# Kernel optimization log

Measured on AMD Instinct MI355X. Metric: run time of the kernel, lower is better.

Reference implementation:

```python
import jax, jax.numpy as jnp
import numpy as np

D_IN, D_MODEL = 512, 256
B, N = 2, 512


def setup_inputs() -> dict:
    key = jax.random.key(0)
    ks = jax.random.split(key, 8)
    xav_x = float(np.sqrt(2.0 / (D_IN + D_MODEL)))
    xav_p = float(np.sqrt(2.0 / (4 + D_MODEL)))
    return {
        "x": jax.random.normal(ks[0], (B, N, D_IN), dtype=jnp.float32),
        "pos": jax.random.normal(ks[1], (B, N, 4), dtype=jnp.float32),
        "attn_mask": jax.random.randint(ks[2], (B, N, N), 0, 2, dtype=jnp.int32),
        "Wx": jax.random.normal(ks[3], (D_IN, D_MODEL), dtype=jnp.float32) * xav_x,
        "bx": jnp.zeros((D_MODEL,), dtype=jnp.float32),
        "Wp": jax.random.normal(ks[4], (4, D_MODEL), dtype=jnp.float32) * xav_p,
        "bp": jnp.zeros((D_MODEL,), dtype=jnp.float32),
        "w": jax.random.normal(ks[5], (D_MODEL,), dtype=jnp.float32) * 0.05,
    }


def reference(x, pos, attn_mask, Wx, bx, Wp, bp, w):
    # projected, activated inputs: [B, N, d_model]
    h = jnp.tanh(x @ Wx + bx)
    # pairwise relative positions: [B, N, N, 4]
    rel = pos[:, :, None, :] - pos[:, None, :, :]
    # position MLP + tanh: [B, N, N, d_model]
    z = jnp.tanh(rel @ Wp + bp)
    # scores via dot with weight vector: [B, N, N]
    attn = jnp.einsum("bijd,d->bij", z, w)
    mask = attn_mask != 0
    attn = jnp.where(mask, attn, -jnp.inf)
    attn = jax.nn.softmax(attn, axis=2)
    attn = jnp.where(mask, attn, 0.0)
    # dropout is identity in eval mode
    # weighted sum: [B, N, d_model]
    output = jnp.einsum("bij,bjd->bid", attn, h)
    return (output, attn)
```

## Files before the change

### kernel.cpp

```cpp
#include <hip/hip_runtime.h>
#include <hip/hip_bf16.h>
#include <math.h>

#define BATCH   2
#define SEQ     512
#define DIN     512
#define DM      256

#define LOG2E2  2.88539008177792681f

#if __has_builtin(__builtin_amdgcn_exp2f)
#define EXP2(x) __builtin_amdgcn_exp2f(x)
#else
#define EXP2(x) exp2f(x)
#endif
#if __has_builtin(__builtin_amdgcn_rcpf)
#define RCP(x) __builtin_amdgcn_rcpf(x)
#else
#define RCP(x) (1.0f / (x))
#endif

__device__ __forceinline__ float tanh_from_scaled(float targ) {
    return fmaf(-2.0f, RCP(1.0f + EXP2(targ)), 1.0f);
}

__global__ __launch_bounds__(512) void prep_k(
    const float* __restrict__ pos,
    const float* __restrict__ Wp,
    const float* __restrict__ bp,
    const float* __restrict__ x,
    const float* __restrict__ Wx,
    const float* __restrict__ bx,
    float* __restrict__ EA,
    float2* __restrict__ EB2,
    float* __restrict__ h)
{
    const int tid = threadIdx.x;

    if (blockIdx.x < 256) {
        const int b  = blockIdx.x >> 7;
        const int tg = blockIdx.x & 127;
        const int d0 = 2 * tg, d1 = d0 + 1;

        const float4 p = ((const float4*)pos)[b * SEQ + tid];
        const float P0 = fmaf(p.x, Wp[d0], fmaf(p.y, Wp[DM + d0],
                         fmaf(p.z, Wp[2*DM + d0], p.w * Wp[3*DM + d0])));
        const float P1 = fmaf(p.x, Wp[d1], fmaf(p.y, Wp[DM + d1],
                         fmaf(p.z, Wp[2*DM + d1], p.w * Wp[3*DM + d1])));
        EB2[((size_t)(b * 128 + tg)) * SEQ + tid] =
            make_float2(EXP2(-LOG2E2 * P0), EXP2(-LOG2E2 * P1));
        return;
    }

    __shared__ float4 s_x[2][DIN/4];
    __shared__ float4 s_part[2][7][64];

    const int row0 = (blockIdx.x - 256) * 2;

    {
        const int r2  = __builtin_amdgcn_readfirstlane(tid >> 8);
        const int d   = tid & 255;
        const int row = row0 + r2;
        const float4 p = ((const float4*)pos)[row];
        const float P = fmaf(p.x, Wp[d],
                        fmaf(p.y, Wp[DM + d],
                        fmaf(p.z, Wp[2*DM + d],
                             p.w * Wp[3*DM + d])));
        EA[(size_t)row * DM + d] = EXP2(LOG2E2 * (P + bp[d]));
    }

    if (tid < 256) {
        const int r   = tid >> 7;
        const int idx = tid & 127;
        s_x[r][idx] = ((const float4*)(x + (size_t)(row0 + r) * DIN))[idx];
    }
    __syncthreads();

    const int w = tid >> 6;
    const int l = tid & 63;

    float4 acc0 = make_float4(0.f, 0.f, 0.f, 0.f);
    float4 acc1 = make_float4(0.f, 0.f, 0.f, 0.f);
    const float* __restrict__ wxp = Wx + 4 * l;

    #pragma unroll 2
    for (int k4 = 0; k4 < 16; k4++) {
        const int kk = w * 16 + k4;
        const float4 xv0 = s_x[0][kk];
        const float4 xv1 = s_x[1][kk];
        const float4 w0 = *(const float4*)(wxp + (size_t)(4*kk + 0) * DM);
        const float4 w1 = *(const float4*)(wxp + (size_t)(4*kk + 1) * DM);
        const float4 w2 = *(const float4*)(wxp + (size_t)(4*kk + 2) * DM);
        const float4 w3 = *(const float4*)(wxp + (size_t)(4*kk + 3) * DM);
        acc0.x = fmaf(xv0.x, w0.x, acc0.x); acc0.y = fmaf(xv0.x, w0.y, acc0.y);
        acc0.z = fmaf(xv0.x, w0.z, acc0.z); acc0.w = fmaf(xv0.x, w0.w, acc0.w);
        acc0.x = fmaf(xv0.y, w1.x, acc0.x); acc0.y = fmaf(xv0.y, w1.y, acc0.y);
        acc0.z = fmaf(xv0.y, w1.z, acc0.z); acc0.w = fmaf(xv0.y, w1.w, acc0.w);
        acc0.x = fmaf(xv0.z, w2.x, acc0.x); acc0.y = fmaf(xv0.z, w2.y, acc0.y);
        acc0.z = fmaf(xv0.z, w2.z, acc0.z); acc0.w = fmaf(xv0.z, w2.w, acc0.w);
        acc0.x = fmaf(xv0.w, w3.x, acc0.x); acc0.y = fmaf(xv0.w, w3.y, acc0.y);
        acc0.z = fmaf(xv0.w, w3.z, acc0.z); acc0.w = fmaf(xv0.w, w3.w, acc0.w);
        acc1.x = fmaf(xv1.x, w0.x, acc1.x); acc1.y = fmaf(xv1.x, w0.y, acc1.y);
        acc1.z = fmaf(xv1.x, w0.z, acc1.z); acc1.w = fmaf(xv1.x, w0.w, acc1.w);
        acc1.x = fmaf(xv1.y, w1.x, acc1.x); acc1.y = fmaf(xv1.y, w1.y, acc1.y);
        acc1.z = fmaf(xv1.y, w1.z, acc1.z); acc1.w = fmaf(xv1.y, w1.w, acc1.w);
        acc1.x = fmaf(xv1.z, w2.x, acc1.x); acc1.y = fmaf(xv1.z, w2.y, acc1.y);
        acc1.z = fmaf(xv1.z, w2.z, acc1.z); acc1.w = fmaf(xv1.z, w2.w, acc1.w);
        acc1.x = fmaf(xv1.w, w3.x, acc1.x); acc1.y = fmaf(xv1.w, w3.y, acc1.y);
        acc1.z = fmaf(xv1.w, w3.z, acc1.z); acc1.w = fmaf(xv1.w, w3.w, acc1.w);
    }

    if (w) {
        s_part[0][w - 1][l] = acc0;
        s_part[1][w - 1][l] = acc1;
    }
    __syncthreads();
    if (w == 0) {
        const float4 b4 = ((const float4*)bx)[l];
        acc0.x += b4.x; acc0.y += b4.y; acc0.z += b4.z; acc0.w += b4.w;
        acc1.x += b4.x; acc1.y += b4.y; acc1.z += b4.z; acc1.w += b4.w;
        #pragma unroll
        for (int q = 0; q < 7; q++) {
            const float4 q0 = s_part[0][q][l];
            const float4 q1 = s_part[1][q][l];
            acc0.x += q0.x; acc0.y += q0.y; acc0.z += q0.z; acc0.w += q0.w;
            acc1.x += q1.x; acc1.y += q1.y; acc1.z += q1.z; acc1.w += q1.w;
        }
        float4 t0, t1;
        t0.x = tanh_from_scaled(LOG2E2 * acc0.x);
        t0.y = tanh_from_scaled(LOG2E2 * acc0.y);
        t0.z = tanh_from_scaled(LOG2E2 * acc0.z);
        t0.w = tanh_from_scaled(LOG2E2 * acc0.w);
        t1.x = tanh_from_scaled(LOG2E2 * acc1.x);
        t1.y = tanh_from_scaled(LOG2E2 * acc1.y);
        t1.z = tanh_from_scaled(LOG2E2 * acc1.z);
        t1.w = tanh_from_scaled(LOG2E2 * acc1.w);
        ((float4*)(h + (size_t)row0 * DM))[l]       = t0;
        ((float4*)(h + (size_t)(row0 + 1) * DM))[l] = t1;
    }
}

__global__ __launch_bounds__(512) void score_k(
    const int*   __restrict__ mask,
    const float* __restrict__ wv,
    const float* __restrict__ EA,
    const float2* __restrict__ EB2,
    float* __restrict__ attn_out)
{
    const int b   = blockIdx.x >> 8;
    const int i0  = (blockIdx.x & 255) * 2;
    const int tid = threadIdx.x;
    const int l   = tid & 63;

    __shared__ float4 s_ea[128];
    __shared__ float  s_red[2][8];

    if (tid < 128) {
        const float2 ea_a = *(const float2*)(EA + (size_t)(b * SEQ + i0) * DM + 2*tid);
        const float2 ea_b = *(const float2*)(EA + (size_t)(b * SEQ + i0 + 1) * DM + 2*tid);
        s_ea[tid] = make_float4(ea_a.x, ea_a.y, ea_b.x, ea_b.y);
    }
    __syncthreads();

    const float2* __restrict__ EBj = EB2 + (size_t)b * 128 * SEQ + tid;

    float aA = 0.f, aB = 0.f;
    #pragma unroll 8
    for (int t = 0; t < 128; t++) {
        const float2 eb = EBj[(size_t)t * SEQ];
        const float4 q  = s_ea[t];
        const float  w0 = wv[2*t];
        const float  w1 = wv[2*t + 1];
        const float yA0 = fmaf(q.x, eb.x, 1.0f);
        const float yA1 = fmaf(q.y, eb.y, 1.0f);
        const float yB0 = fmaf(q.z, eb.x, 1.0f);
        const float yB1 = fmaf(q.w, eb.y, 1.0f);
        aA = fmaf(fmaf(w1, yA0, w0 * yA1), RCP(yA0 * yA1), aA);
        aB = fmaf(fmaf(w1, yB0, w0 * yB1), RCP(yB0 * yB1), aB);
    }

    const size_t mrowA = (size_t)b * SEQ * SEQ + (size_t)i0 * SEQ + tid;
    const int mA = mask[mrowA];
    const int mB = mask[mrowA + SEQ];
    float pA = mA ? EXP2(-LOG2E2 * aA) : 0.f;
    float pB = mB ? EXP2(-LOG2E2 * aB) : 0.f;

    float sA = pA, sB = pB;
    #pragma unroll
    for (int off = 32; off; off >>= 1) {
        sA += __shfl_xor(sA, off, 64);
        sB += __shfl_xor(sB, off, 64);
    }
    const int w = tid >> 6;
    if (l == 0) { s_red[0][w] = sA; s_red[1][w] = sB; }
    __syncthreads();

    const float4 ra = ((const float4*)s_red[0])[0], rb = ((const float4*)s_red[0])[1];
    const float4 rc = ((const float4*)s_red[1])[0], rd = ((const float4*)s_red[1])[1];
    pA *= __fdividef(1.0f, (ra.x+ra.y+ra.z+ra.w) + (rb.x+rb.y+rb.z+rb.w));
    pB *= __fdividef(1.0f, (rc.x+rc.y+rc.z+rc.w) + (rd.x+rd.y+rd.z+rd.w));

    attn_out[mrowA]       = pA;
    attn_out[mrowA + SEQ] = pB;
}

__global__ __launch_bounds__(512) void av_k(
    const float* __restrict__ attn_out,
    const float* __restrict__ h,
    float* __restrict__ out)
{
    const int b   = blockIdx.x >> 8;
    const int i0  = (blockIdx.x & 255) * 2;
    const int tid = threadIdx.x;
    const int jh  = __builtin_amdgcn_readfirstlane(tid >> 8);
    const int d   = tid & 255;

    __shared__ float s_o[2][DM];

    const float* __restrict__ hp  = h + (size_t)(b * SEQ + jh * 256) * DM + d;
    const float* __restrict__ ar0 = attn_out + (size_t)b * SEQ * SEQ
                                  + (size_t)i0 * SEQ + jh * 256;
    const float* __restrict__ ar1 = ar0 + SEQ;

    float c0 = 0.f, c1 = 0.f;
    #pragma unroll 4
    for (int q = 0; q < 64; q++) {
        const float4 P0 = *(const float4*)(ar0 + 4*q);
        const float4 P1 = *(const float4*)(ar1 + 4*q);
        const float h0 = hp[(size_t)(4*q + 0) * DM];
        const float h1 = hp[(size_t)(4*q + 1) * DM];
        const float h2 = hp[(size_t)(4*q + 2) * DM];
        const float h3 = hp[(size_t)(4*q + 3) * DM];
        c0 = fmaf(P0.x, h0, fmaf(P0.y, h1, fmaf(P0.z, h2, fmaf(P0.w, h3, c0))));
        c1 = fmaf(P1.x, h0, fmaf(P1.y, h1, fmaf(P1.z, h2, fmaf(P1.w, h3, c1))));
    }

    if (jh == 1) {
        s_o[0][d] = c0;
        s_o[1][d] = c1;
    }
    __syncthreads();
    if (jh == 0) {
        float* __restrict__ op = out + (size_t)(b * SEQ + i0) * DM + d;
        op[0]  = c0 + s_o[0][d];
        op[DM] = c1 + s_o[1][d];
    }
}

extern "C" void kernel_launch(void* const* d_in, const int* in_sizes, int n_in,
                              void* d_out, int out_size, void* d_ws, size_t ws_size,
                              hipStream_t stream) {
    const float* x    = (const float*)d_in[0];
    const float* pos  = (const float*)d_in[1];
    const int*   mask = (const int*)  d_in[2];
    const float* Wx   = (const float*)d_in[3];
    const float* bx   = (const float*)d_in[4];
    const float* Wp   = (const float*)d_in[5];
    const float* bp   = (const float*)d_in[6];
    const float* wv   = (const float*)d_in[7];

    float* out      = (float*)d_out;
    float* attn_out = (float*)d_out + (size_t)BATCH*SEQ*DM;

    char*   ws  = (char*)d_ws;
    float*  h   = (float*)(ws);
    float*  EA  = (float*)(ws + (size_t)BATCH*SEQ*DM*4);
    float2* EB2 = (float2*)(ws + 2*(size_t)BATCH*SEQ*DM*4);

    prep_k <<<256 + (BATCH*SEQ)/2, 512, 0, stream>>>(pos, Wp, bp, x, Wx, bx, EA, EB2, h);
    score_k<<<(BATCH*SEQ)/2, 512, 0, stream>>>(mask, wv, EA, EB2, attn_out);
    av_k   <<<(BATCH*SEQ)/2, 512, 0, stream>>>(attn_out, h, out);
}
```

Measured before the change: 111.7 us.

## Split prep kernel, tile h GEMM in LDS, widen score and AV loads

Splits the fused prep kernel into a position-exponential kernel and a separate shared-memory tiled GEMM for h (32x32 output tiles, 64-wide K slabs). The score kernel switches EB to float4 packing so each load carries four feature columns. The AV kernel handles four query rows per block with float4 h loads and an eight-way split over j reduced through LDS. The goal is better reuse of Wx and h and fewer, wider memory transactions, at the cost of one extra kernel launch and more LDS reduction traffic.

Measured after the change: 114.5 us. +2.5%, slower.

```diff
diff --git a/kernel.cpp b/kernel.cpp
--- a/kernel.cpp
+++ b/kernel.cpp
@@ -24,127 +24,105 @@
     return fmaf(-2.0f, RCP(1.0f + EXP2(targ)), 1.0f);
 }
 
-__global__ __launch_bounds__(512) void prep_k(
+__global__ __launch_bounds__(512) void pre_k(
     const float* __restrict__ pos,
     const float* __restrict__ Wp,
     const float* __restrict__ bp,
+    float* __restrict__ EA,
+    float4* __restrict__ EB4)
+{
+    const int tid = threadIdx.x;
+
+    if (blockIdx.x < 128) {
+        const int b  = blockIdx.x >> 6;
+        const int q  = blockIdx.x & 63;
+        const int d0 = 4 * q;
+        const float4 p = ((const float4*)pos)[b * SEQ + tid];
+        float e[4];
+        #pragma unroll
+        for (int i = 0; i < 4; i++) {
+            const int d = d0 + i;
+            const float P = fmaf(p.x, Wp[d], fmaf(p.y, Wp[DM + d],
+                            fmaf(p.z, Wp[2*DM + d], p.w * Wp[3*DM + d])));
+            e[i] = EXP2(-LOG2E2 * P);
+        }
+        EB4[((size_t)(b * 64 + q)) * SEQ + tid] = make_float4(e[0], e[1], e[2], e[3]);
+        return;
+    }
+
+    const int idx = blockIdx.x - 128;
+    const int r2  = __builtin_amdgcn_readfirstlane(tid >> 8);
+    const int d   = tid & 255;
+    const int row = idx * 2 + r2;
+    const float4 p = ((const float4*)pos)[row];
+    const float P = fmaf(p.x, Wp[d],
+                    fmaf(p.y, Wp[DM + d],
+                    fmaf(p.z, Wp[2*DM + d],
+                         p.w * Wp[3*DM + d])));
+    EA[(size_t)row * DM + d] = EXP2(LOG2E2 * (P + bp[d]));
+}
+
+__global__ __launch_bounds__(256) void h_k(
     const float* __restrict__ x,
     const float* __restrict__ Wx,
     const float* __restrict__ bx,
-    float* __restrict__ EA,
-    float2* __restrict__ EB2,
     float* __restrict__ h)
 {
-    const int tid = threadIdx.x;
-
-    if (blockIdx.x < 256) {
-        const int b  = blockIdx.x >> 7;
-        const int tg = blockIdx.x & 127;
-        const int d0 = 2 * tg, d1 = d0 + 1;
-
-        const float4 p = ((const float4*)pos)[b * SEQ + tid];
-        const float P0 = fmaf(p.x, Wp[d0], fmaf(p.y, Wp[DM + d0],
-                         fmaf(p.z, Wp[2*DM + d0], p.w * Wp[3*DM + d0])));
-        const float P1 = fmaf(p.x, Wp[d1], fmaf(p.y, Wp[DM + d1],
-                         fmaf(p.z, Wp[2*DM + d1], p.w * Wp[3*DM + d1])));
-        EB2[((size_t)(b * 128 + tg)) * SEQ + tid] =
-            make_float2(EXP2(-LOG2E2 * P0), EXP2(-LOG2E2 * P1));
-        return;
-    }
-
-    __shared__ float4 s_x[2][DIN/4];
-    __shared__ float4 s_part[2][7][64];
-
-    const int row0 = (blockIdx.x - 256) * 2;
-
-    {
-        const int r2  = __builtin_amdgcn_readfirstlane(tid >> 8);
-        const int d   = tid & 255;
-        const int row = row0 + r2;
-        const float4 p = ((const float4*)pos)[row];
-        const float P = fmaf(p.x, Wp[d],
-                        fmaf(p.y, Wp[DM + d],
-                        fmaf(p.z, Wp[2*DM + d],
-                             p.w * Wp[3*DM + d])));
-        EA[(size_t)row * DM + d] = EXP2(LOG2E2 * (P + bp[d]));
-    }
-
-    if (tid < 256) {
-        const int r   = tid >> 7;
-        const int idx = tid & 127;
-        s_x[r][idx] = ((const float4*)(x + (size_t)(row0 + r) * DIN))[idx];
-    }
-    __syncthreads();
-
-    const int w = tid >> 6;
-    const int l = tid & 63;
-
-    float4 acc0 = make_float4(0.f, 0.f, 0.f, 0.f);
-    float4 acc1 = make_float4(0.f, 0.f, 0.f, 0.f);
-    const float* __restrict__ wxp = Wx + 4 * l;
-
-    #pragma unroll 2
-    for (int k4 = 0; k4 < 16; k4++) {
-        const int kk = w * 16 + k4;
-        const float4 xv0 = s_x[0][kk];
-        const float4 xv1 = s_x[1][kk];
-        const float4 w0 = *(const float4*)(wxp + (size_t)(4*kk + 0) * DM);
-        const float4 w1 = *(const float4*)(wxp + (size_t)(4*kk + 1) * DM);
-        const float4 w2 = *(const float4*)(wxp + (size_t)(4*kk + 2) * DM);
-        const float4 w3 = *(const float4*)(wxp + (size_t)(4*kk + 3) * DM);
-        acc0.x = fmaf(xv0.x, w0.x, acc0.x); acc0.y = fmaf(xv0.x, w0.y, acc0.y);
-        acc0.z = fmaf(xv0.x, w0.z, acc0.z); acc0.w = fmaf(xv0.x, w0.w, acc0.w);
-        acc0.x = fmaf(xv0.y, w1.x, acc0.x); acc0.y = fmaf(xv0.y, w1.y, acc0.y);
-        acc0.z = fmaf(xv0.y, w1.z, acc0.z); acc0.w = fmaf(xv0.y, w1.w, acc0.w);
-        acc0.x = fmaf(xv0.z, w2.x, acc0.x); acc0.y = fmaf(xv0.z, w2.y, acc0.y);
-        acc0.z = fmaf(xv0.z, w2.z, acc0.z); acc0.w = fmaf(xv0.z, w2.w, acc0.w);
-        acc0.x = fmaf(xv0.w, w3.x, acc0.x); acc0.y = fmaf(xv0.w, w3.y, acc0.y);
-        acc0.z = fmaf(xv0.w, w3.z, acc0.z); acc0.w = fmaf(xv0.w, w3.w, acc0.w);
-        acc1.x = fmaf(xv1.x, w0.x, acc1.x); acc1.y = fmaf(xv1.x, w0.y, acc1.y);
-        acc1.z = fmaf(xv1.x, w0.z, acc1.z); acc1.w = fmaf(xv1.x, w0.w, acc1.w);
-        acc1.x = fmaf(xv1.y, w1.x, acc1.x); acc1.y = fmaf(xv1.y, w1.y, acc1.y);
-        acc1.z = fmaf(xv1.y, w1.z, acc1.z); acc1.w = fmaf(xv1.y, w1.w, acc1.w);
-        acc1.x = fmaf(xv1.z, w2.x, acc1.x); acc1.y = fmaf(xv1.z, w2.y, acc1.y);
-        acc1.z = fmaf(xv1.z, w2.z, acc1.z); acc1.w = fmaf(xv1.z, w2.w, acc1.w);
-        acc1.x = fmaf(xv1.w, w3.x, acc1.x); acc1.y = fmaf(xv1.w, w3.y, acc1.y);
-        acc1.z = fmaf(xv1.w, w3.z, acc1.z); acc1.w = fmaf(xv1.w, w3.w, acc1.w);
-    }
-
-    if (w) {
-        s_part[0][w - 1][l] = acc0;
-        s_part[1][w - 1][l] = acc1;
-    }
-    __syncthreads();
-    if (w == 0) {
-        const float4 b4 = ((const float4*)bx)[l];
-        acc0.x += b4.x; acc0.y += b4.y; acc0.z += b4.z; acc0.w += b4.w;
-        acc1.x += b4.x; acc1.y += b4.y; acc1.z += b4.z; acc1.w += b4.w;
-        #pragma unroll
-        for (int q = 0; q < 7; q++) {
-            const float4 q0 = s_part[0][q][l];
-            const float4 q1 = s_part[1][q][l];
-            acc0.x += q0.x; acc0.y += q0.y; acc0.z += q0.z; acc0.w += q0.w;
-            acc1.x += q1.x; acc1.y += q1.y; acc1.z += q1.z; acc1.w += q1.w;
-        }
-        float4 t0, t1;
-        t0.x = tanh_from_scaled(LOG2E2 * acc0.x);
-        t0.y = tanh_from_scaled(LOG2E2 * acc0.y);
-        t0.z = tanh_from_scaled(LOG2E2 * acc0.z);
-        t0.w = tanh_from_scaled(LOG2E2 * acc0.w);
-        t1.x = tanh_from_scaled(LOG2E2 * acc1.x);
-        t1.y = tanh_from_scaled(LOG2E2 * acc1.y);
-        t1.z = tanh_from_scaled(LOG2E2 * acc1.z);
-        t1.w = tanh_from_scaled(LOG2E2 * acc1.w);
-        ((float4*)(h + (size_t)row0 * DM))[l]       = t0;
-        ((float4*)(h + (size_t)(row0 + 1) * DM))[l] = t1;
-    }
+    __shared__ float s_xt[32][68];
+    __shared__ float s_wt[64][32];
+
+    const int tid = threadIdx.x;
+    const int rt  = blockIdx.x >> 3;
+    const int ct  = blockIdx.x & 7;
+    const int tx  = tid & 7;
+    const int ty  = tid >> 3;
+
+    float4 acc = make_float4(0.f, 0.f, 0.f, 0.f);
+
+    for (int ks = 0; ks < 8; ks++) {
+        const int k0 = ks * 64;
+        #pragma unroll
+        for (int s = 0; s < 2; s++) {
+            const int fidx = tid * 2 + s;
+            const int r = fidx >> 4, c = fidx & 15;
+            const float4 v = *(const float4*)(x + (size_t)(rt * 32 + r) * DIN + k0 + 4 * c);
+            *(float4*)&s_xt[r][4 * c] = v;
+        }
+        #pragma unroll
+        for (int s = 0; s < 2; s++) {
+            const int fidx = tid * 2 + s;
+            const int r = fidx >> 3, c = fidx & 7;
+            *(float4*)&s_wt[r][4 * c] =
+                *(const float4*)(Wx + (size_t)(k0 + r) * DM + ct * 32 + 4 * c);
+        }
+        __syncthreads();
+
+        #pragma unroll 8
+        for (int k = 0; k < 64; k++) {
+            const float  xv = s_xt[ty][k];
+            const float4 wq = *(const float4*)&s_wt[k][4 * tx];
+            acc.x = fmaf(xv, wq.x, acc.x);
+            acc.y = fmaf(xv, wq.y, acc.y);
+            acc.z = fmaf(xv, wq.z, acc.z);
+            acc.w = fmaf(xv, wq.w, acc.w);
+        }
+        __syncthreads();
+    }
+
+    const float4 bq = *(const float4*)(bx + ct * 32 + 4 * tx);
+    float4 t;
+    t.x = tanh_from_scaled(LOG2E2 * (acc.x + bq.x));
+    t.y = tanh_from_scaled(LOG2E2 * (acc.y + bq.y));
+    t.z = tanh_from_scaled(LOG2E2 * (acc.z + bq.z));
+    t.w = tanh_from_scaled(LOG2E2 * (acc.w + bq.w));
+    *(float4*)(h + (size_t)(rt * 32 + ty) * DM + ct * 32 + 4 * tx) = t;
 }
 
 __global__ __launch_bounds__(512) void score_k(
     const int*   __restrict__ mask,
     const float* __restrict__ wv,
     const float* __restrict__ EA,
-    const float2* __restrict__ EB2,
+    const float4* __restrict__ EB4,
     float* __restrict__ attn_out)
 {
     const int b   = blockIdx.x >> 8;
@@ -152,31 +130,39 @@
     const int tid = threadIdx.x;
     const int l   = tid & 63;
 
-    __shared__ float4 s_ea[128];
+    __shared__ float4 s_eaA[64], s_eaB[64];
     __shared__ float  s_red[2][8];
 
-    if (tid < 128) {
-        const float2 ea_a = *(const float2*)(EA + (size_t)(b * SEQ + i0) * DM + 2*tid);
-        const float2 ea_b = *(const float2*)(EA + (size_t)(b * SEQ + i0 + 1) * DM + 2*tid);
-        s_ea[tid] = make_float4(ea_a.x, ea_a.y, ea_b.x, ea_b.y);
+    if (tid < 64) {
+        s_eaA[tid] = *(const float4*)(EA + (size_t)(b * SEQ + i0) * DM + 4 * tid);
+    } else if (tid < 128) {
+        s_eaB[tid - 64] = *(const float4*)(EA + (size_t)(b * SEQ + i0 + 1) * DM + 4 * (tid - 64));
     }
     __syncthreads();
 
-    const float2* __restrict__ EBj = EB2 + (size_t)b * 128 * SEQ + tid;
+    const float4* __restrict__ EBj = EB4 + (size_t)b * 64 * SEQ + tid;
 
     float aA = 0.f, aB = 0.f;
     #pragma unroll 8
-    for (int t = 0; t < 128; t++) {
-        const float2 eb = EBj[(size_t)t * SEQ];
-        const float4 q  = s_ea[t];
-        const float  w0 = wv[2*t];
-        const float  w1 = wv[2*t + 1];
-        const float yA0 = fmaf(q.x, eb.x, 1.0f);
-        const float yA1 = fmaf(q.y, eb.y, 1.0f);
-        const float yB0 = fmaf(q.z, eb.x, 1.0f);
-        const float yB1 = fmaf(q.w, eb.y, 1.0f);
-        aA = fmaf(fmaf(w1, yA0, w0 * yA1), RCP(yA0 * yA1), aA);
-        aB = fmaf(fmaf(w1, yB0, w0 * yB1), RCP(yB0 * yB1), aB);
+    for (int q = 0; q < 64; q++) {
+        const float4 eb = EBj[(size_t)q * SEQ];
+        const float4 eA = s_eaA[q];
+        const float4 eB = s_eaB[q];
+        const float4 wq = *(const float4*)(wv + 4 * q);
+
+        const float yA0 = fmaf(eA.x, eb.x, 1.0f);
+        const float yA1 = fmaf(eA.y, eb.y, 1.0f);
+        const float yA2 = fmaf(eA.z, eb.z, 1.0f);
+        const float yA3 = fmaf(eA.w, eb.w, 1.0f);
+        aA = fmaf(fmaf(wq.y, yA0, wq.x * yA1), RCP(yA0 * yA1), aA);
+        aA = fmaf(fmaf(wq.w, yA2, wq.z * yA3), RCP(yA2 * yA3), aA);
+
+        const float yB0 = fmaf(eB.x, eb.x, 1.0f);
+        const float yB1 = fmaf(eB.y, eb.y, 1.0f);
+        const float yB2 = fmaf(eB.z, eb.z, 1.0f);
+        const float yB3 = fmaf(eB.w, eb.w, 1.0f);
+        aB = fmaf(fmaf(wq.y, yB0, wq.x * yB1), RCP(yB0 * yB1), aB);
+        aB = fmaf(fmaf(wq.w, yB2, wq.z * yB3), RCP(yB2 * yB3), aB);
     }
 
     const size_t mrowA = (size_t)b * SEQ * SEQ + (size_t)i0 * SEQ + tid;
@@ -209,41 +195,75 @@
     const float* __restrict__ h,
     float* __restrict__ out)
 {
-    const int b   = blockIdx.x >> 8;
-    const int i0  = (blockIdx.x & 255) * 2;
-    const int tid = threadIdx.x;
-    const int jh  = __builtin_amdgcn_readfirstlane(tid >> 8);
-    const int d   = tid & 255;
-
-    __shared__ float s_o[2][DM];
-
-    const float* __restrict__ hp  = h + (size_t)(b * SEQ + jh * 256) * DM + d;
+    const int b   = blockIdx.x >> 7;
+    const int i0  = (blockIdx.x & 127) * 4;
+    const int tid = threadIdx.x;
+    const int dq  = tid & 63;
+    const int js  = __builtin_amdgcn_readfirstlane(tid >> 6);
+
+    __shared__ float s_av[7][4][DM];
+
+    const float* __restrict__ hp = h + (size_t)(b * SEQ + js * 64) * DM + 4 * dq;
     const float* __restrict__ ar0 = attn_out + (size_t)b * SEQ * SEQ
-                                  + (size_t)i0 * SEQ + jh * 256;
+                                  + (size_t)i0 * SEQ + js * 64;
     const float* __restrict__ ar1 = ar0 + SEQ;
-
-    float c0 = 0.f, c1 = 0.f;
+    const float* __restrict__ ar2 = ar0 + 2 * SEQ;
+    const float* __restrict__ ar3 = ar0 + 3 * SEQ;
+
+    float4 a0 = make_float4(0,0,0,0), a1 = a0, a2 = a0, a3 = a0;
     #pragma unroll 4
-    for (int q = 0; q < 64; q++) {
-        const float4 P0 = *(const float4*)(ar0 + 4*q);
-        const float4 P1 = *(const float4*)(ar1 + 4*q);
-        const float h0 = hp[(size_t)(4*q + 0) * DM];
-        const float h1 = hp[(size_t)(4*q + 1) * DM];
-        const float h2 = hp[(size_t)(4*q + 2) * DM];
-        const float h3 = hp[(size_t)(4*q + 3) * DM];
-        c0 = fmaf(P0.x, h0, fmaf(P0.y, h1, fmaf(P0.z, h2, fmaf(P0.w, h3, c0))));
-        c1 = fmaf(P1.x, h0, fmaf(P1.y, h1, fmaf(P1.z, h2, fmaf(P1.w, h3, c1))));
-    }
-
-    if (jh == 1) {
-        s_o[0][d] = c0;
-        s_o[1][d] = c1;
+    for (int jj = 0; jj < 16; jj++) {
+        const float4 P0 = *(const float4*)(ar0 + 4 * jj);
+        const float4 P1 = *(const float4*)(ar1 + 4 * jj);
+        const float4 P2 = *(const float4*)(ar2 + 4 * jj);
+        const float4 P3 = *(const float4*)(ar3 + 4 * jj);
+        const float4 h0 = *(const float4*)(hp + (size_t)(4*jj + 0) * DM);
+        const float4 h1 = *(const float4*)(hp + (size_t)(4*jj + 1) * DM);
+        const float4 h2 = *(const float4*)(hp + (size_t)(4*jj + 2) * DM);
+        const float4 h3 = *(const float4*)(hp + (size_t)(4*jj + 3) * DM);
+
+        a0.x = fmaf(P0.x,h0.x,fmaf(P0.y,h1.x,fmaf(P0.z,h2.x,fmaf(P0.w,h3.x,a0.x))));
+        a0.y = fmaf(P0.x,h0.y,fmaf(P0.y,h1.y,fmaf(P0.z,h2.y,fmaf(P0.w,h3.y,a0.y))));
+        a0.z = fmaf(P0.x,h0.z,fmaf(P0.y,h1.z,fmaf(P0.z,h2.z,fmaf(P0.w,h3.z,a0.z))));
+        a0.w = fmaf(P0.x,h0.w,fmaf(P0.y,h1.w,fmaf(P0.z,h2.w,fmaf(P0.w,h3.w,a0.w))));
+        a1.x = fmaf(P1.x,h0.x,fmaf(P1.y,h1.x,fmaf(P1.z,h2.x,fmaf(P1.w,h3.x,a1.x))));
+        a1.y = fmaf(P1.x,h0.y,fmaf(P1.y,h1.y,fmaf(P1.z,h2.y,fmaf(P1.w,h3.y,a1.y))));
+        a1.z = fmaf(P1.x,h0.z,fmaf(P1.y,h1.z,fmaf(P1.z,h2.z,fmaf(P1.w,h3.z,a1.z))));
+        a1.w = fmaf(P1.x,h0.w,fmaf(P1.y,h1.w,fmaf(P1.z,h2.w,fmaf(P1.w,h3.w,a1.w))));
+        a2.x = fmaf(P2.x,h0.x,fmaf(P2.y,h1.x,fmaf(P2.z,h2.x,fmaf(P2.w,h3.x,a2.x))));
+        a2.y = fmaf(P2.x,h0.y,fmaf(P2.y,h1.y,fmaf(P2.z,h2.y,fmaf(P2.w,h3.y,a2.y))));
+        a2.z = fmaf(P2.x,h0.z,fmaf(P2.y,h1.z,fmaf(P2.z,h2.z,fmaf(P2.w,h3.z,a2.z))));
+        a2.w = fmaf(P2.x,h0.w,fmaf(P2.y,h1.w,fmaf(P2.z,h2.w,fmaf(P2.w,h3.w,a2.w))));
+        a3.x = fmaf(P3.x,h0.x,fmaf(P3.y,h1.x,fmaf(P3.z,h2.x,fmaf(P3.w,h3.x,a3.x))));
+        a3.y = fmaf(P3.x,h0.y,fmaf(P3.y,h1.y,fmaf(P3.z,h2.y,fmaf(P3.w,h3.y,a3.y))));
+        a3.z = fmaf(P3.x,h0.z,fmaf(P3.y,h1.z,fmaf(P3.z,h2.z,fmaf(P3.w,h3.z,a3.z))));
+        a3.w = fmaf(P3.x,h0.w,fmaf(P3.y,h1.w,fmaf(P3.z,h2.w,fmaf(P3.w,h3.w,a3.w))));
+    }
+
+    if (js > 0) {
+        *(float4*)&s_av[js - 1][0][4 * dq] = a0;
+        *(float4*)&s_av[js - 1][1][4 * dq] = a1;
+        *(float4*)&s_av[js - 1][2][4 * dq] = a2;
+        *(float4*)&s_av[js - 1][3][4 * dq] = a3;
     }
     __syncthreads();
-    if (jh == 0) {
-        float* __restrict__ op = out + (size_t)(b * SEQ + i0) * DM + d;
-        op[0]  = c0 + s_o[0][d];
-        op[DM] = c1 + s_o[1][d];
+    if (js == 0) {
+        #pragma unroll
+        for (int s = 0; s < 7; s++) {
+            const float4 q0 = *(const float4*)&s_av[s][0][4 * dq];
+            const float4 q1 = *(const float4*)&s_av[s][1][4 * dq];
+            const float4 q2 = *(const float4*)&s_av[s][2][4 * dq];
+            const float4 q3 = *(const float4*)&s_av[s][3][4 * dq];
+            a0.x += q0.x; a0.y += q0.y; a0.z += q0.z; a0.w += q0.w;
+            a1.x += q1.x; a1.y += q1.y; a1.z += q1.z; a1.w += q1.w;
+            a2.x += q2.x; a2.y += q2.y; a2.z += q2.z; a2.w += q2.w;
+            a3.x += q3.x; a3.y += q3.y; a3.z += q3.z; a3.w += q3.w;
+        }
+        float* __restrict__ op = out + (size_t)(b * SEQ + i0) * DM + 4 * dq;
+        *(float4*)(op)          = a0;
+        *(float4*)(op + DM)     = a1;
+        *(float4*)(op + 2*DM)   = a2;
+        *(float4*)(op + 3*DM)   = a3;
     }
 }
 
@@ -265,9 +285,10 @@
     char*   ws  = (char*)d_ws;
     float*  h   = (float*)(ws);
     float*  EA  = (float*)(ws + (size_t)BATCH*SEQ*DM*4);
-    float2* EB2 = (float2*)(ws + 2*(size_t)BATCH*SEQ*DM*4);
-
-    prep_k <<<256 + (BATCH*SEQ)/2, 512, 0, stream>>>(pos, Wp, bp, x, Wx, bx, EA, EB2, h);
-    score_k<<<(BATCH*SEQ)/2, 512, 0, stream>>>(mask, wv, EA, EB2, attn_out);
-    av_k   <<<(BATCH*SEQ)/2, 512, 0, stream>>>(attn_out, h, out);
-}
+    float4* EB4 = (float4*)(ws + 2*(size_t)BATCH*SEQ*DM*4);
+
+    pre_k  <<<128 + (BATCH*SEQ)/2, 512, 0, stream>>>(pos, Wp, bp, EA, EB4);
+    h_k    <<<256, 256, 0, stream>>>(x, Wx, bx, h);
+    score_k<<<(BATCH*SEQ)/2, 512, 0, stream>>>(mask, wv, EA, EB4, attn_out);
+    av_k   <<<(BATCH*SEQ)/4, 512, 0, stream>>>(attn_out, h, out);
+}
```
